# Optimization experiments

Measured on AMD Instinct MI355X. Metric: run time of the kernel, lower is better.

Reference implementation:

```python
import jax, jax.numpy as jnp
import numpy as np

N_NODES = 50000
NNZ = 800000
NUM_EDGES = 10000
D = 128
EPS = 1e-8


def setup_inputs() -> dict:
    key = jax.random.key(0)
    k1, k2, k3, k4 = jax.random.split(key, 4)
    x = jax.random.normal(k1, (N_NODES, D), dtype=jnp.float32)
    node_ids = jax.random.randint(k2, (NNZ,), 0, N_NODES, dtype=jnp.int64)
    edge_ids = jax.random.randint(k3, (NNZ,), 0, NUM_EDGES, dtype=jnp.int64)
    hyperedge_index = jnp.stack([node_ids, edge_ids], axis=0)  # [2, nnz]
    # nn.Linear(in, out, bias=False) weight is [out, in]; kaiming-uniform-ish init
    bound = 1.0 / np.sqrt(D)
    W_node = jax.random.uniform(k4, (D, D), minval=-bound, maxval=bound, dtype=jnp.float32)
    bias = jnp.zeros((D,), dtype=jnp.float32)
    return {"x": x, "hyperedge_index": hyperedge_index, "W_node": W_node,
            "bias": bias, "num_hyperedges": NUM_EDGES}


def reference(x, hyperedge_index, W_node, bias, num_hyperedges):
    src = hyperedge_index[0]   # node ids, [nnz]
    edge = hyperedge_index[1]  # hyperedge ids, [nnz]
    N = x.shape[0]

    x_node = x @ W_node.T                                # [N, D]

    # node -> hyperedge mean
    edge_sum = jax.ops.segment_sum(x_node[src], edge, num_segments=num_hyperedges)
    node_counts = jax.ops.segment_sum(jnp.ones_like(edge, dtype=x.dtype), edge,
                                      num_segments=num_hyperedges)
    hyperedge_attr = edge_sum / (node_counts[:, None] + EPS)  # [E, D]

    # hyperedge -> node mean
    out = jax.ops.segment_sum(hyperedge_attr[edge], src, num_segments=N)
    degrees = jax.ops.segment_sum(jnp.ones_like(src, dtype=x.dtype), src,
                                  num_segments=N)
    out = out / (degrees[:, None] + EPS)                 # [N, D]

    return out + x_node + bias
```

## Files before the change

### kernel.cpp

```cpp
#include <hip/hip_runtime.h>

#define D 128
#define EPS 1e-8f
#define E_NUM 10000
#define CAP_E 192
#define CAP_N 64
#define CHUNK 2048
#define EB2 2500
#define NB2 782
#define TB 3282
#define CAPB_E 512
#define CAPB_N 1280
#define NODE_BASE (EB2 * CAPB_E)
#define STAGE_TOTAL (NODE_BASE + NB2 * CAPB_N)

typedef __attribute__((ext_vector_type(8))) short bf16x8;
typedef __attribute__((ext_vector_type(4))) float f32x4;

__device__ __forceinline__ unsigned bf16rn(float f) {
  unsigned u = __float_as_uint(f);
  return (u + 0x7fffu + ((u >> 16) & 1u)) >> 16;
}
__device__ __forceinline__ unsigned bf16pack(float a, float b) {
  return bf16rn(a) | (bf16rn(b) << 16);
}
__device__ __forceinline__ float lof(unsigned u) { return __uint_as_float(u << 16); }
__device__ __forceinline__ float hif(unsigned u) { return __uint_as_float(u & 0xffff0000u); }

#define ACCQ(u) do { \
    x0 += lof((u).x); y0 += hif((u).x); x1 += lof((u).y); y1 += hif((u).y); \
    x2 += lof((u).z); y2 += hif((u).z); x3 += lof((u).w); y3 += hif((u).w); } while (0)

struct SmemGemm {
  unsigned short Wfrag[2048 * 8];
  unsigned short cbuf[4][16 * 136];
};
struct SmemScat {
  int h[TB];
  int cur[TB];
  int end_[TB];
};

__global__ __launch_bounds__(256) void k1_gemm_scatter(
    const float* __restrict__ x, const float* __restrict__ W,
    unsigned* __restrict__ xnb, const int* __restrict__ node_ids,
    const int* __restrict__ edge_ids, int* __restrict__ gcur,
    unsigned* __restrict__ stage, int nnz, int C, int N) {
  __shared__ union { SmemGemm g; SmemScat s; } sm;
  const int t = threadIdx.x;

  if ((int)blockIdx.x < C) {
    const int c = blockIdx.x;
    const int base = c * CHUNK;
    const int lim = min(base + CHUNK, nnz);
    unsigned pk[8], rk[8];
    #pragma unroll
    for (int r = 0; r < 8; ++r) {
      int i = base + t + r * 256;
      pk[r] = (i < lim)
          ? (((unsigned)edge_ids[i] << 16) | (unsigned)node_ids[i])
          : 0xffffffffu;
    }
    for (int j = t; j < TB; j += 256) sm.s.h[j] = 0;
    __syncthreads();
    #pragma unroll
    for (int r = 0; r < 8; ++r) {
      if (pk[r] != 0xffffffffu) {
        unsigned pe = atomicAdd(&sm.s.h[pk[r] >> 18], 1);
        unsigned pn = atomicAdd(&sm.s.h[EB2 + ((pk[r] & 0xffffu) >> 6)], 1);
        rk[r] = pe | (pn << 16);
      } else {
        rk[r] = 0;
      }
    }
    __syncthreads();
    for (int j = t; j < TB; j += 256) {
      int hc = sm.s.h[j];
      int rb, cap;
      if (j < EB2) { rb = j * CAPB_E; cap = CAPB_E; }
      else         { rb = NODE_BASE + (j - EB2) * CAPB_N; cap = CAPB_N; }
      int off = hc ? atomicAdd(&gcur[j], hc) : 0;
      sm.s.cur[j] = rb + off;
      sm.s.end_[j] = rb + cap;
    }
    __syncthreads();
    #pragma unroll
    for (int r = 0; r < 8; ++r) {
      if (pk[r] != 0xffffffffu) {
        int be = pk[r] >> 18;
        int bn = EB2 + ((pk[r] & 0xffffu) >> 6);
        int pe = sm.s.cur[be] + (int)(rk[r] & 0xffffu);
        if (pe < sm.s.end_[be]) stage[pe] = pk[r];
        int pn = sm.s.cur[bn] + (int)(rk[r] >> 16);
        if (pn < sm.s.end_[bn]) stage[pn] = (pk[r] << 16) | (pk[r] >> 16);
      }
    }
    return;
  }

  const int wid = t >> 6;
  const int lane = t & 63;
  const int m = lane & 15;
  const int q = lane >> 4;

  #pragma unroll
  for (int i = 0; i < 8; ++i) {
    int c2 = t + i * 256;
    int ctkt = c2 >> 6;
    int l2 = c2 & 63;
    int n = (ctkt >> 2) * 16 + (l2 & 15);
    int k = (ctkt & 3) * 32 + (l2 >> 4) * 8;
    float4 p = *(const float4*)&W[n * 128 + k];
    float4 r = *(const float4*)&W[n * 128 + k + 4];
    uint4 pkk = make_uint4(bf16pack(p.x, p.y), bf16pack(p.z, p.w),
                           bf16pack(r.x, r.y), bf16pack(r.z, r.w));
    *(uint4*)&sm.g.Wfrag[c2 * 8] = pkk;
  }
  __syncthreads();

  const int blockRow = (blockIdx.x - C) * 128;
  #pragma unroll
  for (int s = 0; s < 2; ++s) {
    const int row0 = blockRow + wid * 32 + s * 16;
    if (row0 >= N) break;

    bf16x8 a[4];
    #pragma unroll
    for (int kt = 0; kt < 4; ++kt) {
      int k0 = kt * 32 + q * 8;
      float4 p = *(const float4*)&x[(size_t)(row0 + m) * 128 + k0];
      float4 r = *(const float4*)&x[(size_t)(row0 + m) * 128 + k0 + 4];
      union { bf16x8 v; uint4 u; } au;
      au.u = make_uint4(bf16pack(p.x, p.y), bf16pack(p.z, p.w),
                        bf16pack(r.x, r.y), bf16pack(r.z, r.w));
      a[kt] = au.v;
    }

    #pragma unroll
    for (int ct = 0; ct < 8; ++ct) {
      f32x4 acc = {0.f, 0.f, 0.f, 0.f};
      #pragma unroll
      for (int kt = 0; kt < 4; ++kt) {
        bf16x8 b = *(const bf16x8*)&sm.g.Wfrag[((ct * 4 + kt) * 64 + lane) * 8];
        acc = __builtin_amdgcn_mfma_f32_16x16x32_bf16(a[kt], b, acc, 0, 0, 0);
      }
      #pragma unroll
      for (int r = 0; r < 4; ++r)
        sm.g.cbuf[wid][(q * 4 + r) * 136 + ct * 16 + m] =
            (unsigned short)bf16rn(acc[r]);
    }

    #pragma unroll
    for (int pass = 0; pass < 4; ++pass) {
      int chunk = pass * 64 + lane;
      int row = chunk >> 4;
      int cc = chunk & 15;
      uint4 v = *(const uint4*)&sm.g.cbuf[wid][row * 136 + cc * 8];
      *(uint4*)&xnb[(size_t)(row0 + row) * 64 + cc * 4] = v;
    }
  }
}

__global__ __launch_bounds__(256) void fuse_edge(
    const unsigned* __restrict__ stage, const int* __restrict__ gcur,
    const unsigned* __restrict__ xnb, unsigned* __restrict__ eattr) {
  __shared__ __align__(16) unsigned short lists[4 * CAP_E];
  __shared__ int lc[4];
  int b = blockIdx.x, t = threadIdx.x;
  if (t < 4) lc[t] = 0;
  __syncthreads();
  int total = gcur[b];
  if (total > CAPB_E) total = CAPB_E;
  const unsigned* seg = stage + (size_t)b * CAPB_E;
  for (int i = t; i < total; i += 256) {
    unsigned pkv = seg[i];
    int e = pkv >> 16;
    int p = atomicAdd(&lc[e & 3], 1);
    if (p < CAP_E) lists[(e & 3) * CAP_E + p] = (unsigned short)(pkv & 0xffffu);
  }
  __syncthreads();

  const int wid = t >> 6, lane = t & 63;
  const int h2 = lane >> 4, w = lane & 15;
  const uint4* X4 = (const uint4*)xnb;
  const int j = wid;
  const int e = (b << 2) + j;
  int c = lc[j];
  if (c > CAP_E) c = CAP_E;
  const unsigned short* lst = &lists[j * CAP_E];
  float x0=0,y0=0,x1=0,y1=0,x2=0,y2=0,x3=0,y3=0;
  int m2 = 0;
  uint4 a0, a1, a2, a3;
  if (m2 + 16 <= c) {
    a0 = X4[(size_t)lst[m2 + h2] * 16 + w];
    a1 = X4[(size_t)lst[m2 + 4 + h2] * 16 + w];
    a2 = X4[(size_t)lst[m2 + 8 + h2] * 16 + w];
    a3 = X4[(size_t)lst[m2 + 12 + h2] * 16 + w];
  }
  for (; m2 + 32 <= c; m2 += 16) {
    uint4 b0 = X4[(size_t)lst[m2 + 16 + h2] * 16 + w];
    uint4 b1 = X4[(size_t)lst[m2 + 20 + h2] * 16 + w];
    uint4 b2 = X4[(size_t)lst[m2 + 24 + h2] * 16 + w];
    uint4 b3 = X4[(size_t)lst[m2 + 28 + h2] * 16 + w];
    ACCQ(a0); ACCQ(a1); ACCQ(a2); ACCQ(a3);
    a0 = b0; a1 = b1; a2 = b2; a3 = b3;
  }
  if (m2 + 16 <= c) {
    ACCQ(a0); ACCQ(a1); ACCQ(a2); ACCQ(a3);
    m2 += 16;
  }
  for (; m2 < c; m2 += 4) {
    int ii = m2 + h2;
    int id = lst[ii < c ? ii : m2];
    uint4 u = X4[(size_t)id * 16 + w];
    if (ii < c) ACCQ(u);
  }
  x0 += __shfl_xor(x0, 16); y0 += __shfl_xor(y0, 16);
  x1 += __shfl_xor(x1, 16); y1 += __shfl_xor(y1, 16);
  x2 += __shfl_xor(x2, 16); y2 += __shfl_xor(y2, 16);
  x3 += __shfl_xor(x3, 16); y3 += __shfl_xor(y3, 16);
  x0 += __shfl_xor(x0, 32); y0 += __shfl_xor(y0, 32);
  x1 += __shfl_xor(x1, 32); y1 += __shfl_xor(y1, 32);
  x2 += __shfl_xor(x2, 32); y2 += __shfl_xor(y2, 32);
  x3 += __shfl_xor(x3, 32); y3 += __shfl_xor(y3, 32);
  if (lane < 16) {
    float inv = 1.f / ((float)c + EPS);
    uint4 o = make_uint4(bf16pack(x0 * inv, y0 * inv), bf16pack(x1 * inv, y1 * inv),
                         bf16pack(x2 * inv, y2 * inv), bf16pack(x3 * inv, y3 * inv));
    ((uint4*)eattr)[(size_t)e * 16 + w] = o;
  }
}

__global__ __launch_bounds__(512) void fuse_node(
    const unsigned* __restrict__ stage, const int* __restrict__ gcur,
    const unsigned* __restrict__ eattr, const unsigned* __restrict__ xnb,
    const float* __restrict__ bias, float* __restrict__ out, int N) {
  __shared__ __align__(16) unsigned short lists[64 * CAP_N];
  __shared__ int lc[64];
  int b = blockIdx.x, t = threadIdx.x;
  if (t < 64) lc[t] = 0;
  __syncthreads();
  int total = gcur[EB2 + b];
  if (total > CAPB_N) total = CAPB_N;
  const unsigned* seg = stage + NODE_BASE + (size_t)b * CAPB_N;
  for (int i = t; i < total; i += 512) {
    unsigned pkv = seg[i];
    int n = pkv >> 16;
    int p = atomicAdd(&lc[n & 63], 1);
    if (p < CAP_N) lists[(n & 63) * CAP_N + p] = (unsigned short)(pkv & 0xffffu);
  }
  __syncthreads();

  const int wid = t >> 6, lane = t & 63;
  const int h2 = lane >> 4, w = lane & 15;
  const uint4* E4 = (const uint4*)eattr;
  const float4* B4 = (const float4*)bias;
  float4 bv0 = B4[2 * w], bv1 = B4[2 * w + 1];
  #pragma unroll
  for (int rep = 0; rep < 8; ++rep) {
    int j = wid + rep * 8;
    int v = (b << 6) + j;
    if (v >= N) continue;
    int c = lc[j];
    if (c > CAP_N) c = CAP_N;
    const unsigned short* lst = &lists[j * CAP_N];
    float x0=0,y0=0,x1=0,y1=0,x2=0,y2=0,x3=0,y3=0;
    int m2 = 0;
    for (; m2 + 16 <= c; m2 += 16) {
      int i0 = lst[m2 + h2],     i1 = lst[m2 + 4 + h2],
          i2 = lst[m2 + 8 + h2], i3 = lst[m2 + 12 + h2];
      uint4 u0 = E4[(size_t)i0 * 16 + w];
      uint4 u1 = E4[(size_t)i1 * 16 + w];
      uint4 u2 = E4[(size_t)i2 * 16 + w];
      uint4 u3 = E4[(size_t)i3 * 16 + w];
      ACCQ(u0); ACCQ(u1); ACCQ(u2); ACCQ(u3);
    }
    for (; m2 < c; m2 += 4) {
      int ii = m2 + h2;
      int id = lst[ii < c ? ii : m2];
      uint4 u = E4[(size_t)id * 16 + w];
      if (ii < c) ACCQ(u);
    }
    x0 += __shfl_xor(x0, 16); y0 += __shfl_xor(y0, 16);
    x1 += __shfl_xor(x1, 16); y1 += __shfl_xor(y1, 16);
    x2 += __shfl_xor(x2, 16); y2 += __shfl_xor(y2, 16);
    x3 += __shfl_xor(x3, 16); y3 += __shfl_xor(y3, 16);
    x0 += __shfl_xor(x0, 32); y0 += __shfl_xor(y0, 32);
    x1 += __shfl_xor(x1, 32); y1 += __shfl_xor(y1, 32);
    x2 += __shfl_xor(x2, 32); y2 += __shfl_xor(y2, 32);
    x3 += __shfl_xor(x3, 32); y3 += __shfl_xor(y3, 32);
    if (lane < 16) {
      float inv = 1.f / ((float)c + EPS);
      uint4 xr = ((const uint4*)xnb)[(size_t)v * 16 + w];
      float4 o0 = make_float4(x0 * inv + lof(xr.x) + bv0.x,
                              y0 * inv + hif(xr.x) + bv0.y,
                              x1 * inv + lof(xr.y) + bv0.z,
                              y1 * inv + hif(xr.y) + bv0.w);
      float4 o1 = make_float4(x2 * inv + lof(xr.z) + bv1.x,
                              y2 * inv + hif(xr.z) + bv1.y,
                              x3 * inv + lof(xr.w) + bv1.z,
                              y3 * inv + hif(xr.w) + bv1.w);
      float4* orow = (float4*)(out + (size_t)v * D);
      orow[2 * w] = o0;
      orow[2 * w + 1] = o1;
    }
  }
}

extern "C" void kernel_launch(void* const* d_in, const int* in_sizes, int n_in,
                              void* d_out, int out_size, void* d_ws, size_t ws_size,
                              hipStream_t stream) {
  const float* x = (const float*)d_in[0];
  const int* hidx = (const int*)d_in[1];
  const float* W = (const float*)d_in[2];
  const float* bias = (const float*)d_in[3];

  const int N = in_sizes[0] / D;
  const int nnz = in_sizes[1] / 2;
  const int* node_ids = hidx;
  const int* edge_ids = hidx + nnz;
  const int C = (nnz + CHUNK - 1) / CHUNK;
  const int GB = (N + 127) / 128;

  int* ib = (int*)d_ws;
  int* gcur = ib;
  unsigned* stage = (unsigned*)(ib + 4096);
  unsigned* xnb = (unsigned*)(ib + 4096 + STAGE_TOTAL);
  unsigned* eattr = xnb + (size_t)N * 64;

  (void)hipMemsetAsync(gcur, 0, TB * sizeof(int), stream);

  k1_gemm_scatter<<<C + GB, 256, 0, stream>>>(x, W, xnb, node_ids, edge_ids,
                                              gcur, stage, nnz, C, N);

  fuse_edge<<<EB2, 256, 0, stream>>>(stage, gcur, xnb, eattr);

  fuse_node<<<NB2, 512, 0, stream>>>(stage, gcur, eattr, xnb, bias,
                                     (float*)d_out, N);
}
```

Before: 168.5 us.

## Build per-edge and per-node adjacency lists directly with global atomics

Replaces the two-level bucketed staging scheme (a shared-memory histogram, bucket reservation and a staged scatter, then per-block list rebuilding in shared memory) with direct per-edge and per-node fixed-capacity lists filled by global atomicAdd. The fuse kernels then read their list straight from global memory, one wave per edge or node, with no shared-memory rebuild and smaller blocks for the node pass. This removes a pass over the staged data and the in-kernel sorting. In exchange it issues 1.6M global atomics on contended counters and scatters 2-byte writes across memory, which may cost more than the staged approach.

```diff
diff --git a/kernel.cpp b/kernel.cpp
--- a/kernel.cpp
+++ b/kernel.cpp
@@ -6,13 +6,6 @@
 #define CAP_E 192
 #define CAP_N 64
 #define CHUNK 2048
-#define EB2 2500
-#define NB2 782
-#define TB 3282
-#define CAPB_E 512
-#define CAPB_N 1280
-#define NODE_BASE (EB2 * CAPB_E)
-#define STAGE_TOTAL (NODE_BASE + NB2 * CAPB_N)
 
 typedef __attribute__((ext_vector_type(8))) short bf16x8;
 typedef __attribute__((ext_vector_type(4))) float f32x4;
@@ -35,65 +28,26 @@
   unsigned short Wfrag[2048 * 8];
   unsigned short cbuf[4][16 * 136];
 };
-struct SmemScat {
-  int h[TB];
-  int cur[TB];
-  int end_[TB];
-};
-
-__global__ __launch_bounds__(256) void k1_gemm_scatter(
+
+__global__ __launch_bounds__(256) void k1_gemm_build(
     const float* __restrict__ x, const float* __restrict__ W,
     unsigned* __restrict__ xnb, const int* __restrict__ node_ids,
-    const int* __restrict__ edge_ids, int* __restrict__ gcur,
-    unsigned* __restrict__ stage, int nnz, int C, int N) {
-  __shared__ union { SmemGemm g; SmemScat s; } sm;
+    const int* __restrict__ edge_ids, int* __restrict__ ecnt,
+    int* __restrict__ ncnt, unsigned short* __restrict__ elist,
+    unsigned short* __restrict__ nlist, int nnz, int LB, int N) {
+  __shared__ SmemGemm g;
   const int t = threadIdx.x;
 
-  if ((int)blockIdx.x < C) {
-    const int c = blockIdx.x;
-    const int base = c * CHUNK;
+  if ((int)blockIdx.x < LB) {
+    const int base = (int)blockIdx.x * CHUNK;
     const int lim = min(base + CHUNK, nnz);
-    unsigned pk[8], rk[8];
-    #pragma unroll
-    for (int r = 0; r < 8; ++r) {
-      int i = base + t + r * 256;
-      pk[r] = (i < lim)
-          ? (((unsigned)edge_ids[i] << 16) | (unsigned)node_ids[i])
-          : 0xffffffffu;
-    }
-    for (int j = t; j < TB; j += 256) sm.s.h[j] = 0;
-    __syncthreads();
-    #pragma unroll
-    for (int r = 0; r < 8; ++r) {
-      if (pk[r] != 0xffffffffu) {
-        unsigned pe = atomicAdd(&sm.s.h[pk[r] >> 18], 1);
-        unsigned pn = atomicAdd(&sm.s.h[EB2 + ((pk[r] & 0xffffu) >> 6)], 1);
-        rk[r] = pe | (pn << 16);
-      } else {
-        rk[r] = 0;
-      }
-    }
-    __syncthreads();
-    for (int j = t; j < TB; j += 256) {
-      int hc = sm.s.h[j];
-      int rb, cap;
-      if (j < EB2) { rb = j * CAPB_E; cap = CAPB_E; }
-      else         { rb = NODE_BASE + (j - EB2) * CAPB_N; cap = CAPB_N; }
-      int off = hc ? atomicAdd(&gcur[j], hc) : 0;
-      sm.s.cur[j] = rb + off;
-      sm.s.end_[j] = rb + cap;
-    }
-    __syncthreads();
-    #pragma unroll
-    for (int r = 0; r < 8; ++r) {
-      if (pk[r] != 0xffffffffu) {
-        int be = pk[r] >> 18;
-        int bn = EB2 + ((pk[r] & 0xffffu) >> 6);
-        int pe = sm.s.cur[be] + (int)(rk[r] & 0xffffu);
-        if (pe < sm.s.end_[be]) stage[pe] = pk[r];
-        int pn = sm.s.cur[bn] + (int)(rk[r] >> 16);
-        if (pn < sm.s.end_[bn]) stage[pn] = (pk[r] << 16) | (pk[r] >> 16);
-      }
+    for (int i = base + t; i < lim; i += 256) {
+      int e = edge_ids[i];
+      int n = node_ids[i];
+      int pe = atomicAdd(&ecnt[e], 1);
+      if (pe < CAP_E) elist[(size_t)e * CAP_E + pe] = (unsigned short)n;
+      int pn = atomicAdd(&ncnt[n], 1);
+      if (pn < CAP_N) nlist[(size_t)n * CAP_N + pn] = (unsigned short)e;
     }
     return;
   }
@@ -114,11 +68,11 @@
     float4 r = *(const float4*)&W[n * 128 + k + 4];
     uint4 pkk = make_uint4(bf16pack(p.x, p.y), bf16pack(p.z, p.w),
                            bf16pack(r.x, r.y), bf16pack(r.z, r.w));
-    *(uint4*)&sm.g.Wfrag[c2 * 8] = pkk;
+    *(uint4*)&g.Wfrag[c2 * 8] = pkk;
   }
   __syncthreads();
 
-  const int blockRow = (blockIdx.x - C) * 128;
+  const int blockRow = ((int)blockIdx.x - LB) * 128;
   #pragma unroll
   for (int s = 0; s < 2; ++s) {
     const int row0 = blockRow + wid * 32 + s * 16;
@@ -141,12 +95,12 @@
       f32x4 acc = {0.f, 0.f, 0.f, 0.f};
       #pragma unroll
       for (int kt = 0; kt < 4; ++kt) {
-        bf16x8 b = *(const bf16x8*)&sm.g.Wfrag[((ct * 4 + kt) * 64 + lane) * 8];
+        bf16x8 b = *(const bf16x8*)&g.Wfrag[((ct * 4 + kt) * 64 + lane) * 8];
         acc = __builtin_amdgcn_mfma_f32_16x16x32_bf16(a[kt], b, acc, 0, 0, 0);
       }
       #pragma unroll
       for (int r = 0; r < 4; ++r)
-        sm.g.cbuf[wid][(q * 4 + r) * 136 + ct * 16 + m] =
+        g.cbuf[wid][(q * 4 + r) * 136 + ct * 16 + m] =
             (unsigned short)bf16rn(acc[r]);
     }
 
@@ -155,47 +109,33 @@
       int chunk = pass * 64 + lane;
       int row = chunk >> 4;
       int cc = chunk & 15;
-      uint4 v = *(const uint4*)&sm.g.cbuf[wid][row * 136 + cc * 8];
+      uint4 v = *(const uint4*)&g.cbuf[wid][row * 136 + cc * 8];
       *(uint4*)&xnb[(size_t)(row0 + row) * 64 + cc * 4] = v;
     }
   }
 }
 
 __global__ __launch_bounds__(256) void fuse_edge(
-    const unsigned* __restrict__ stage, const int* __restrict__ gcur,
+    const int* __restrict__ ecnt, const unsigned short* __restrict__ elist,
     const unsigned* __restrict__ xnb, unsigned* __restrict__ eattr) {
-  __shared__ __align__(16) unsigned short lists[4 * CAP_E];
-  __shared__ int lc[4];
-  int b = blockIdx.x, t = threadIdx.x;
-  if (t < 4) lc[t] = 0;
-  __syncthreads();
-  int total = gcur[b];
-  if (total > CAPB_E) total = CAPB_E;
-  const unsigned* seg = stage + (size_t)b * CAPB_E;
-  for (int i = t; i < total; i += 256) {
-    unsigned pkv = seg[i];
-    int e = pkv >> 16;
-    int p = atomicAdd(&lc[e & 3], 1);
-    if (p < CAP_E) lists[(e & 3) * CAP_E + p] = (unsigned short)(pkv & 0xffffu);
-  }
-  __syncthreads();
-
+  const int t = threadIdx.x;
   const int wid = t >> 6, lane = t & 63;
   const int h2 = lane >> 4, w = lane & 15;
+  const int e = (int)blockIdx.x * 4 + wid;
+  if (e >= E_NUM) return;
+
   const uint4* X4 = (const uint4*)xnb;
-  const int j = wid;
-  const int e = (b << 2) + j;
-  int c = lc[j];
+  int c = ecnt[e];
   if (c > CAP_E) c = CAP_E;
-  const unsigned short* lst = &lists[j * CAP_E];
+  const unsigned short* lst = elist + (size_t)e * CAP_E;
   float x0=0,y0=0,x1=0,y1=0,x2=0,y2=0,x3=0,y3=0;
   int m2 = 0;
   uint4 a0, a1, a2, a3;
-  if (m2 + 16 <= c) {
-    a0 = X4[(size_t)lst[m2 + h2] * 16 + w];
-    a1 = X4[(size_t)lst[m2 + 4 + h2] * 16 + w];
-    a2 = X4[(size_t)lst[m2 + 8 + h2] * 16 + w];
-    a3 = X4[(size_t)lst[m2 + 12 + h2] * 16 + w];
+  if (c >= 16) {
+    a0 = X4[(size_t)lst[h2] * 16 + w];
+    a1 = X4[(size_t)lst[4 + h2] * 16 + w];
+    a2 = X4[(size_t)lst[8 + h2] * 16 + w];
+    a3 = X4[(size_t)lst[12 + h2] * 16 + w];
   }
   for (; m2 + 32 <= c; m2 += 16) {
     uint4 b0 = X4[(size_t)lst[m2 + 16 + h2] * 16 + w];
@@ -231,79 +171,59 @@
   }
 }
 
-__global__ __launch_bounds__(512) void fuse_node(
-    const unsigned* __restrict__ stage, const int* __restrict__ gcur,
+__global__ __launch_bounds__(256) void fuse_node(
+    const int* __restrict__ ncnt, const unsigned short* __restrict__ nlist,
     const unsigned* __restrict__ eattr, const unsigned* __restrict__ xnb,
     const float* __restrict__ bias, float* __restrict__ out, int N) {
-  __shared__ __align__(16) unsigned short lists[64 * CAP_N];
-  __shared__ int lc[64];
-  int b = blockIdx.x, t = threadIdx.x;
-  if (t < 64) lc[t] = 0;
-  __syncthreads();
-  int total = gcur[EB2 + b];
-  if (total > CAPB_N) total = CAPB_N;
-  const unsigned* seg = stage + NODE_BASE + (size_t)b * CAPB_N;
-  for (int i = t; i < total; i += 512) {
-    unsigned pkv = seg[i];
-    int n = pkv >> 16;
-    int p = atomicAdd(&lc[n & 63], 1);
-    if (p < CAP_N) lists[(n & 63) * CAP_N + p] = (unsigned short)(pkv & 0xffffu);
-  }
-  __syncthreads();
-
+  const int t = threadIdx.x;
   const int wid = t >> 6, lane = t & 63;
   const int h2 = lane >> 4, w = lane & 15;
+  const int v = (int)blockIdx.x * 4 + wid;
+  if (v >= N) return;
+
   const uint4* E4 = (const uint4*)eattr;
   const float4* B4 = (const float4*)bias;
   float4 bv0 = B4[2 * w], bv1 = B4[2 * w + 1];
-  #pragma unroll
-  for (int rep = 0; rep < 8; ++rep) {
-    int j = wid + rep * 8;
-    int v = (b << 6) + j;
-    if (v >= N) continue;
-    int c = lc[j];
-    if (c > CAP_N) c = CAP_N;
-    const unsigned short* lst = &lists[j * CAP_N];
-    float x0=0,y0=0,x1=0,y1=0,x2=0,y2=0,x3=0,y3=0;
-    int m2 = 0;
-    for (; m2 + 16 <= c; m2 += 16) {
-      int i0 = lst[m2 + h2],     i1 = lst[m2 + 4 + h2],
-          i2 = lst[m2 + 8 + h2], i3 = lst[m2 + 12 + h2];
-      uint4 u0 = E4[(size_t)i0 * 16 + w];
-      uint4 u1 = E4[(size_t)i1 * 16 + w];
-      uint4 u2 = E4[(size_t)i2 * 16 + w];
-      uint4 u3 = E4[(size_t)i3 * 16 + w];
-      ACCQ(u0); ACCQ(u1); ACCQ(u2); ACCQ(u3);
-    }
-    for (; m2 < c; m2 += 4) {
-      int ii = m2 + h2;
-      int id = lst[ii < c ? ii : m2];
-      uint4 u = E4[(size_t)id * 16 + w];
-      if (ii < c) ACCQ(u);
-    }
-    x0 += __shfl_xor(x0, 16); y0 += __shfl_xor(y0, 16);
-    x1 += __shfl_xor(x1, 16); y1 += __shfl_xor(y1, 16);
-    x2 += __shfl_xor(x2, 16); y2 += __shfl_xor(y2, 16);
-    x3 += __shfl_xor(x3, 16); y3 += __shfl_xor(y3, 16);
-    x0 += __shfl_xor(x0, 32); y0 += __shfl_xor(y0, 32);
-    x1 += __shfl_xor(x1, 32); y1 += __shfl_xor(y1, 32);
-    x2 += __shfl_xor(x2, 32); y2 += __shfl_xor(y2, 32);
-    x3 += __shfl_xor(x3, 32); y3 += __shfl_xor(y3, 32);
-    if (lane < 16) {
-      float inv = 1.f / ((float)c + EPS);
-      uint4 xr = ((const uint4*)xnb)[(size_t)v * 16 + w];
-      float4 o0 = make_float4(x0 * inv + lof(xr.x) + bv0.x,
-                              y0 * inv + hif(xr.x) + bv0.y,
-                              x1 * inv + lof(xr.y) + bv0.z,
-                              y1 * inv + hif(xr.y) + bv0.w);
-      float4 o1 = make_float4(x2 * inv + lof(xr.z) + bv1.x,
-                              y2 * inv + hif(xr.z) + bv1.y,
-                              x3 * inv + lof(xr.w) + bv1.z,
-                              y3 * inv + hif(xr.w) + bv1.w);
-      float4* orow = (float4*)(out + (size_t)v * D);
-      orow[2 * w] = o0;
-      orow[2 * w + 1] = o1;
-    }
+  int c = ncnt[v];
+  if (c > CAP_N) c = CAP_N;
+  const unsigned short* lst = nlist + (size_t)v * CAP_N;
+  float x0=0,y0=0,x1=0,y1=0,x2=0,y2=0,x3=0,y3=0;
+  int m2 = 0;
+  for (; m2 + 16 <= c; m2 += 16) {
+    uint4 u0 = E4[(size_t)lst[m2 + h2] * 16 + w];
+    uint4 u1 = E4[(size_t)lst[m2 + 4 + h2] * 16 + w];
+    uint4 u2 = E4[(size_t)lst[m2 + 8 + h2] * 16 + w];
+    uint4 u3 = E4[(size_t)lst[m2 + 12 + h2] * 16 + w];
+    ACCQ(u0); ACCQ(u1); ACCQ(u2); ACCQ(u3);
+  }
+  for (; m2 < c; m2 += 4) {
+    int ii = m2 + h2;
+    int id = lst[ii < c ? ii : m2];
+    uint4 u = E4[(size_t)id * 16 + w];
+    if (ii < c) ACCQ(u);
+  }
+  x0 += __shfl_xor(x0, 16); y0 += __shfl_xor(y0, 16);
+  x1 += __shfl_xor(x1, 16); y1 += __shfl_xor(y1, 16);
+  x2 += __shfl_xor(x2, 16); y2 += __shfl_xor(y2, 16);
+  x3 += __shfl_xor(x3, 16); y3 += __shfl_xor(y3, 16);
+  x0 += __shfl_xor(x0, 32); y0 += __shfl_xor(y0, 32);
+  x1 += __shfl_xor(x1, 32); y1 += __shfl_xor(y1, 32);
+  x2 += __shfl_xor(x2, 32); y2 += __shfl_xor(y2, 32);
+  x3 += __shfl_xor(x3, 32); y3 += __shfl_xor(y3, 32);
+  if (lane < 16) {
+    float inv = 1.f / ((float)c + EPS);
+    uint4 xr = ((const uint4*)xnb)[(size_t)v * 16 + w];
+    float4 o0 = make_float4(x0 * inv + lof(xr.x) + bv0.x,
+                            y0 * inv + hif(xr.x) + bv0.y,
+                            x1 * inv + lof(xr.y) + bv0.z,
+                            y1 * inv + hif(xr.y) + bv0.w);
+    float4 o1 = make_float4(x2 * inv + lof(xr.z) + bv1.x,
+                            y2 * inv + hif(xr.z) + bv1.y,
+                            x3 * inv + lof(xr.w) + bv1.z,
+                            y3 * inv + hif(xr.w) + bv1.w);
+    float4* orow = (float4*)(out + (size_t)v * D);
+    orow[2 * w] = o0;
+    orow[2 * w + 1] = o1;
   }
 }
 
@@ -319,22 +239,25 @@
   const int nnz = in_sizes[1] / 2;
   const int* node_ids = hidx;
   const int* edge_ids = hidx + nnz;
-  const int C = (nnz + CHUNK - 1) / CHUNK;
+  const int LB = (nnz + CHUNK - 1) / CHUNK;
   const int GB = (N + 127) / 128;
 
   int* ib = (int*)d_ws;
-  int* gcur = ib;
-  unsigned* stage = (unsigned*)(ib + 4096);
-  unsigned* xnb = (unsigned*)(ib + 4096 + STAGE_TOTAL);
+  int* ecnt = ib;
+  int* ncnt = ib + 10240;
+  unsigned* xnb = (unsigned*)(ib + 61440);
   unsigned* eattr = xnb + (size_t)N * 64;
-
-  (void)hipMemsetAsync(gcur, 0, TB * sizeof(int), stream);
-
-  k1_gemm_scatter<<<C + GB, 256, 0, stream>>>(x, W, xnb, node_ids, edge_ids,
-                                              gcur, stage, nnz, C, N);
-
-  fuse_edge<<<EB2, 256, 0, stream>>>(stage, gcur, xnb, eattr);
-
-  fuse_node<<<NB2, 512, 0, stream>>>(stage, gcur, eattr, xnb, bias,
-                                     (float*)d_out, N);
-}
+  unsigned short* elist = (unsigned short*)(eattr + (size_t)E_NUM * 64);
+  unsigned short* nlist = elist + (size_t)E_NUM * CAP_E;
+
+  (void)hipMemsetAsync(ib, 0, 61440 * sizeof(int), stream);
+
+  k1_gemm_build<<<LB + GB, 256, 0, stream>>>(x, W, xnb, node_ids, edge_ids,
+                                             ecnt, ncnt, elist, nlist,
+                                             nnz, LB, N);
+
+  fuse_edge<<<(E_NUM + 3) / 4, 256, 0, stream>>>(ecnt, elist, xnb, eattr);
+
+  fuse_node<<<(N + 3) / 4, 256, 0, stream>>>(ncnt, nlist, eattr, xnb, bias,
+                                             (float*)d_out, N);
+}
```

New measurement: 228.8 us. 1.36x slower.

## Coarsen edge buckets and split edge listing into separate listify kernel

Applied to the files above, without the earlier changes.

Edge buckets now cover 16 hyperedges instead of 4, which cuts the histogram bucket count and the global atomics in the scatter phase. A new listify_edge kernel sorts each bucket into per-edge node lists in shared memory and writes them back in place into the staging buffer along with per-edge counts. fuse_edge then reads those prebuilt lists straight from global memory with no shared-memory listing step. This adds one kernel launch and an extra pass over the staging buffer, in exchange for fewer atomics and leaner gather blocks.

```diff
diff --git a/kernel.cpp b/kernel.cpp
--- a/kernel.cpp
+++ b/kernel.cpp
@@ -6,10 +6,10 @@
 #define CAP_E 192
 #define CAP_N 64
 #define CHUNK 2048
-#define EB2 2500
+#define EB2 625
 #define NB2 782
-#define TB 3282
-#define CAPB_E 512
+#define TB 1407
+#define CAPB_E 1536
 #define CAPB_N 1280
 #define NODE_BASE (EB2 * CAPB_E)
 #define STAGE_TOTAL (NODE_BASE + NB2 * CAPB_N)
@@ -66,7 +66,7 @@
     #pragma unroll
     for (int r = 0; r < 8; ++r) {
       if (pk[r] != 0xffffffffu) {
-        unsigned pe = atomicAdd(&sm.s.h[pk[r] >> 18], 1);
+        unsigned pe = atomicAdd(&sm.s.h[pk[r] >> 20], 1);
         unsigned pn = atomicAdd(&sm.s.h[EB2 + ((pk[r] & 0xffffu) >> 6)], 1);
         rk[r] = pe | (pn << 16);
       } else {
@@ -87,7 +87,7 @@
     #pragma unroll
     for (int r = 0; r < 8; ++r) {
       if (pk[r] != 0xffffffffu) {
-        int be = pk[r] >> 18;
+        int be = pk[r] >> 20;
         int bn = EB2 + ((pk[r] & 0xffffu) >> 6);
         int pe = sm.s.cur[be] + (int)(rk[r] & 0xffffu);
         if (pe < sm.s.end_[be]) stage[pe] = pk[r];
@@ -118,7 +118,7 @@
   }
   __syncthreads();
 
-  const int blockRow = (blockIdx.x - C) * 128;
+  const int blockRow = ((int)blockIdx.x - C) * 128;
   #pragma unroll
   for (int s = 0; s < 2; ++s) {
     const int row0 = blockRow + wid * 32 + s * 16;
@@ -161,41 +161,53 @@
   }
 }
 
-__global__ __launch_bounds__(256) void fuse_edge(
-    const unsigned* __restrict__ stage, const int* __restrict__ gcur,
-    const unsigned* __restrict__ xnb, unsigned* __restrict__ eattr) {
-  __shared__ __align__(16) unsigned short lists[4 * CAP_E];
-  __shared__ int lc[4];
-  int b = blockIdx.x, t = threadIdx.x;
-  if (t < 4) lc[t] = 0;
+__global__ __launch_bounds__(256) void listify_edge(
+    const int* __restrict__ gcur, unsigned* __restrict__ stage,
+    int* __restrict__ ecnt) {
+  __shared__ unsigned short l16[16][CAP_E];
+  __shared__ int lc[16];
+  const int b = blockIdx.x, t = threadIdx.x;
+  if (t < 16) lc[t] = 0;
   __syncthreads();
   int total = gcur[b];
   if (total > CAPB_E) total = CAPB_E;
-  const unsigned* seg = stage + (size_t)b * CAPB_E;
-  for (int i = t; i < total; i += 256) {
-    unsigned pkv = seg[i];
-    int e = pkv >> 16;
-    int p = atomicAdd(&lc[e & 3], 1);
-    if (p < CAP_E) lists[(e & 3) * CAP_E + p] = (unsigned short)(pkv & 0xffffu);
-  }
-  __syncthreads();
-
+  unsigned* seg = stage + (size_t)b * CAPB_E;
+  #pragma unroll
+  for (int r = 0; r < 6; ++r) {
+    int i = t + r * 256;
+    if (i < total) {
+      unsigned pkv = seg[i];
+      int e = (pkv >> 16) & 15;
+      int p = atomicAdd(&lc[e], 1);
+      if (p < CAP_E) l16[e][p] = (unsigned short)(pkv & 0xffffu);
+    }
+  }
+  __syncthreads();
+  if (t < 16) ecnt[b * 16 + t] = min(lc[t], CAP_E);
+  const unsigned* src = (const unsigned*)l16;
+  for (int i = t; i < 1536; i += 256) seg[i] = src[i];
+}
+
+__global__ __launch_bounds__(256) void fuse_edge(
+    const int* __restrict__ ecnt, const unsigned* __restrict__ stage,
+    const unsigned* __restrict__ xnb, unsigned* __restrict__ eattr) {
+  const int t = threadIdx.x;
   const int wid = t >> 6, lane = t & 63;
   const int h2 = lane >> 4, w = lane & 15;
+  const int e = (int)blockIdx.x * 4 + wid;
   const uint4* X4 = (const uint4*)xnb;
-  const int j = wid;
-  const int e = (b << 2) + j;
-  int c = lc[j];
-  if (c > CAP_E) c = CAP_E;
-  const unsigned short* lst = &lists[j * CAP_E];
+  int c = ecnt[e];
+  const unsigned short* lst =
+      (const unsigned short*)(stage + (size_t)(e >> 4) * CAPB_E) +
+      (e & 15) * CAP_E;
   float x0=0,y0=0,x1=0,y1=0,x2=0,y2=0,x3=0,y3=0;
   int m2 = 0;
   uint4 a0, a1, a2, a3;
-  if (m2 + 16 <= c) {
-    a0 = X4[(size_t)lst[m2 + h2] * 16 + w];
-    a1 = X4[(size_t)lst[m2 + 4 + h2] * 16 + w];
-    a2 = X4[(size_t)lst[m2 + 8 + h2] * 16 + w];
-    a3 = X4[(size_t)lst[m2 + 12 + h2] * 16 + w];
+  if (c >= 16) {
+    a0 = X4[(size_t)lst[h2] * 16 + w];
+    a1 = X4[(size_t)lst[4 + h2] * 16 + w];
+    a2 = X4[(size_t)lst[8 + h2] * 16 + w];
+    a3 = X4[(size_t)lst[12 + h2] * 16 + w];
   }
   for (; m2 + 32 <= c; m2 += 16) {
     uint4 b0 = X4[(size_t)lst[m2 + 16 + h2] * 16 + w];
@@ -267,12 +279,10 @@
     float x0=0,y0=0,x1=0,y1=0,x2=0,y2=0,x3=0,y3=0;
     int m2 = 0;
     for (; m2 + 16 <= c; m2 += 16) {
-      int i0 = lst[m2 + h2],     i1 = lst[m2 + 4 + h2],
-          i2 = lst[m2 + 8 + h2], i3 = lst[m2 + 12 + h2];
-      uint4 u0 = E4[(size_t)i0 * 16 + w];
-      uint4 u1 = E4[(size_t)i1 * 16 + w];
-      uint4 u2 = E4[(size_t)i2 * 16 + w];
-      uint4 u3 = E4[(size_t)i3 * 16 + w];
+      uint4 u0 = E4[(size_t)lst[m2 + h2] * 16 + w];
+      uint4 u1 = E4[(size_t)lst[m2 + 4 + h2] * 16 + w];
+      uint4 u2 = E4[(size_t)lst[m2 + 8 + h2] * 16 + w];
+      uint4 u3 = E4[(size_t)lst[m2 + 12 + h2] * 16 + w];
       ACCQ(u0); ACCQ(u1); ACCQ(u2); ACCQ(u3);
     }
     for (; m2 < c; m2 += 4) {
@@ -324,8 +334,9 @@
 
   int* ib = (int*)d_ws;
   int* gcur = ib;
-  unsigned* stage = (unsigned*)(ib + 4096);
-  unsigned* xnb = (unsigned*)(ib + 4096 + STAGE_TOTAL);
+  int* ecnt = ib + 2048;
+  unsigned* stage = (unsigned*)(ib + 16384);
+  unsigned* xnb = stage + STAGE_TOTAL;
   unsigned* eattr = xnb + (size_t)N * 64;
 
   (void)hipMemsetAsync(gcur, 0, TB * sizeof(int), stream);
@@ -333,7 +344,9 @@
   k1_gemm_scatter<<<C + GB, 256, 0, stream>>>(x, W, xnb, node_ids, edge_ids,
                                               gcur, stage, nnz, C, N);
 
-  fuse_edge<<<EB2, 256, 0, stream>>>(stage, gcur, xnb, eattr);
+  listify_edge<<<EB2, 256, 0, stream>>>(gcur, stage, ecnt);
+
+  fuse_edge<<<(E_NUM + 3) / 4, 256, 0, stream>>>(ecnt, stage, xnb, eattr);
 
   fuse_node<<<NB2, 512, 0, stream>>>(stage, gcur, eattr, xnb, bias,
                                      (float*)d_out, N);
```

Result: no change. 169.6 us (+0.6%).
